# Performance work log

Measured on AMD Instinct MI355X. Metric: run time of the kernel, lower is better.

Reference implementation:

```python
import jax, jax.numpy as jnp
import numpy as np

B, N, C_IN, C_OUT, K = 2, 2048, 64, 128, 3
SCALE = 12.0  # spread points over ~12^3 unit voxels (voxel_size = 1.0 in the module)


def setup_inputs() -> dict:
    key = jax.random.key(0)
    k1, k2, k3 = jax.random.split(key, 3)
    points = jax.random.uniform(k1, (B, N, 3), dtype=jnp.float32) * SCALE
    features = jax.random.normal(k2, (B, N, C_IN), dtype=jnp.float32)
    # kaiming-uniform-ish init for weight viewed as (K^3*Cin, Cout)
    fan_in = K * K * K * C_IN
    bound = np.sqrt(6.0 / fan_in)
    weight = jax.random.uniform(k3, (K, K, K, C_IN, C_OUT), dtype=jnp.float32,
                                minval=-bound, maxval=bound)
    bias = jnp.zeros((C_OUT,), dtype=jnp.float32)
    return {"points": points, "features": features, "weight": weight, "bias": bias}


def reference(points, features, weight, bias):
    """Sparse 3D conv over a unit voxel grid.

    For each point i, every point j whose voxel index differs by an offset
    within the KxKxK stencil contributes features[j] @ weight[rel_offset].
    Vectorized as: per-offset boolean match matrix (B,N,N) -> masked
    feature aggregation -> one GEMM with that offset's (Cin,Cout) kernel slice.
    """
    k = weight.shape[0]
    c = k // 2
    # torch's .long() truncates toward zero; jnp astype(int32) does the same for floats
    vox = points.astype(jnp.int32)  # (B, N, 3)
    out = jnp.zeros(features.shape[:2] + (weight.shape[-1],), dtype=features.dtype)
    for oi in range(k):
        for oj in range(k):
            for ok in range(k):
                off = jnp.array([oi - c, oj - c, ok - c], dtype=jnp.int32)
                target = vox + off  # voxel that neighbor j must occupy for center i
                # mask[b, i, j] = all(vox[b, j] == vox[b, i] + off)
                mask = jnp.all(vox[:, None, :, :] == target[:, :, None, :], axis=-1)
                agg = jnp.einsum('bij,bjc->bic', mask.astype(features.dtype), features)
                out = out + agg @ weight[oi, oj, ok]  # (B,N,Cin)@(Cin,Cout)
    return out + bias
```

## Files before the change

kernel.cpp:

```cpp
#include <hip/hip_runtime.h>

#define BATCH 2
#define NPTS  2048
#define CIN   64
#define COUT  128
#define GD    14
#define GD2   (GD*GD)
#define NCELL (GD*GD*GD)
#define M     (BATCH*NPTS)
#define VOXF  (BATCH*NCELL*CIN)
#define WTEL  (27*COUT*CIN)

typedef __bf16 bf16x8 __attribute__((ext_vector_type(8)));
typedef float  f32x4  __attribute__((ext_vector_type(4)));
typedef unsigned short us8 __attribute__((ext_vector_type(8)));

__device__ __forceinline__ unsigned short f2bf(float f) {
    unsigned u = __builtin_bit_cast(unsigned, f);
    return (unsigned short)((u + 0x7FFFu + ((u >> 16) & 1u)) >> 16);
}

__global__ __launch_bounds__(256) void k_init(const float* __restrict__ points,
                                              const float* __restrict__ weight,
                                              int* __restrict__ abase,
                                              unsigned short* __restrict__ wT) {
    const int t = threadIdx.x;
    if (blockIdx.x < 27) {
        const int off = blockIdx.x;
        __shared__ unsigned short lds[128*65 + 64];
        const float* wsrc = weight + off*8192;
        #pragma unroll
        for (int i = 0; i < 32; ++i) {
            const int s = t + i*256;
            const int k = s >> 7, n = s & 127;
            lds[n*65 + k] = f2bf(wsrc[k*128 + n]);
        }
        __syncthreads();
        unsigned short* wdst = wT + off*8192;
        #pragma unroll
        for (int i = 0; i < 32; ++i) {
            const int s = t + i*256;
            const int n = s >> 6, k = s & 63;
            wdst[n*64 + k] = lds[n*65 + k];
        }
    } else {
        const int g = (blockIdx.x - 27)*256 + t;
        const int vx = (int)points[g*3 + 0];
        const int vy = (int)points[g*3 + 1];
        const int vz = (int)points[g*3 + 2];
        const int cell = (vx + 1)*GD2 + (vy + 1)*GD + (vz + 1);
        abase[g] = ((g >> 11)*NCELL + cell)*CIN;
    }
}

__global__ __launch_bounds__(256) void k_scatter(const float* __restrict__ feat,
                                                 const int* __restrict__ abase,
                                                 float* __restrict__ voxgrid) {
    const int idx = blockIdx.x * 256 + threadIdx.x;
    const int g   = idx >> 6;
    const int cin = idx & 63;
    atomicAdd(&voxgrid[abase[g] + cin], feat[idx]);
}

__global__ __launch_bounds__(256) void k_pack(const float* __restrict__ voxgrid,
                                              unsigned short* __restrict__ voxbf) {
    const int idx = blockIdx.x * 256 + threadIdx.x;
    if (idx >= VOXF/8) return;
    const float4 v0 = ((const float4*)voxgrid)[idx*2 + 0];
    const float4 v1 = ((const float4*)voxgrid)[idx*2 + 1];
    us8 p;
    p[0] = f2bf(v0.x); p[1] = f2bf(v0.y); p[2] = f2bf(v0.z); p[3] = f2bf(v0.w);
    p[4] = f2bf(v1.x); p[5] = f2bf(v1.y); p[6] = f2bf(v1.z); p[7] = f2bf(v1.w);
    *(us8*)(voxbf + idx*8) = p;
}

__global__ __launch_bounds__(256) void k_gemm(const unsigned short* __restrict__ voxbf,
                                              const int* __restrict__ abase,
                                              const unsigned short* __restrict__ wT,
                                              const float* __restrict__ bias,
                                              float* __restrict__ out) {
    static constexpr int DELTA[27] = {
        -211,-210,-209,-197,-196,-195,-183,-182,-181,
         -15, -14, -13,  -1,   0,   1,  13,  14,  15,
         181, 182, 183, 195, 196, 197, 209, 210, 211 };

    const int t   = threadIdx.x;
    const int l   = t & 63;
    const int w   = t >> 6;
    const int q   = l >> 4;
    const int col = l & 15;
    const int g0  = blockIdx.x * 16;
    const int n0  = (blockIdx.y * 4 + w) * 16;

    const int rowoff = abase[g0 + col];
    const unsigned short* arow = voxbf + rowoff + q*8;
    const unsigned short* wtp  = wT + (size_t)(n0 + col)*CIN + q*8;

    f32x4 acc = {0.f, 0.f, 0.f, 0.f};

    us8 A0[3], A1[3], B0[3], B1[3];
    #pragma unroll
    for (int p = 0; p < 3; ++p) {
        const int d = DELTA[p]*CIN;
        A0[p] = *(const us8*)(arow + d);
        A1[p] = *(const us8*)(arow + d + 32);
        B0[p] = *(const us8*)(wtp + p*8192);
        B1[p] = *(const us8*)(wtp + p*8192 + 32);
    }

    #pragma unroll
    for (int oo = 0; oo < 27; ++oo) {
        const int s = oo % 3;
        const us8 a0 = A0[s], a1 = A1[s], b0 = B0[s], b1 = B1[s];
        if (oo + 3 < 27) {
            const int d = DELTA[oo+3]*CIN;
            A0[s] = *(const us8*)(arow + d);
            A1[s] = *(const us8*)(arow + d + 32);
            B0[s] = *(const us8*)(wtp + (oo+3)*8192);
            B1[s] = *(const us8*)(wtp + (oo+3)*8192 + 32);
        }
        acc = __builtin_amdgcn_mfma_f32_16x16x32_bf16(
                  __builtin_bit_cast(bf16x8, a0), __builtin_bit_cast(bf16x8, b0), acc, 0, 0, 0);
        acc = __builtin_amdgcn_mfma_f32_16x16x32_bf16(
                  __builtin_bit_cast(bf16x8, a1), __builtin_bit_cast(bf16x8, b1), acc, 0, 0, 0);
    }

    const float bs = bias[n0 + col];
    #pragma unroll
    for (int r = 0; r < 4; ++r) {
        out[(size_t)(g0 + q*4 + r)*COUT + n0 + col] = acc[r] + bs;
    }
}

extern "C" void kernel_launch(void* const* d_in, const int* in_sizes, int n_in,
                              void* d_out, int out_size, void* d_ws, size_t ws_size,
                              hipStream_t stream) {
    (void)in_sizes; (void)n_in; (void)out_size; (void)ws_size;
    const float* points   = (const float*)d_in[0];
    const float* features = (const float*)d_in[1];
    const float* weight   = (const float*)d_in[2];
    const float* bias     = (const float*)d_in[3];
    float* out = (float*)d_out;

    char* ws = (char*)d_ws;
    float*          voxgrid = (float*)ws;
    int*            abase   = (int*)(ws + 1404928);
    unsigned short* wTp     = (unsigned short*)(ws + 1404928 + 16384);
    unsigned short* voxbf   = (unsigned short*)(ws + 1404928 + 16384 + 442368);

    hipMemsetAsync(voxgrid, 0, (size_t)VOXF*4, stream);
    k_init<<<43, 256, 0, stream>>>(points, weight, abase, wTp);
    k_scatter<<<(M*CIN)/256, 256, 0, stream>>>(features, abase, voxgrid);
    k_pack<<<(VOXF/8 + 255)/256, 256, 0, stream>>>(voxgrid, voxbf);
    dim3 grid(M/16, 2, 1);
    k_gemm<<<grid, 256, 0, stream>>>(voxbf, abase, wTp, bias, out);
}
```

Baseline: 94.87 us.

## Compute conv per voxel cell then gather to points; fuse init and scatter

The GEMM now runs over all 2x1728 occupied-range voxel cells instead of over the 4096 points, writes a dense per-cell output grid, and a new gather kernel copies each point's cell row to the output. The weight is re-laid-out so that the three z-offsets of a stencil row form one contiguous 192-wide K dimension. This lets the A loads for those offsets come from contiguous voxel memory. The separate init and scatter kernels are merged into one prep kernel to save a launch. The trade-off is fewer GEMM rows (3456 vs 4096) in exchange for an extra gather kernel and an extra intermediate buffer round trip.

```diff
diff --git a/kernel.cpp b/kernel.cpp
--- a/kernel.cpp
+++ b/kernel.cpp
@@ -9,7 +9,7 @@
 #define NCELL (GD*GD*GD)
 #define M     (BATCH*NPTS)
 #define VOXF  (BATCH*NCELL*CIN)
-#define WTEL  (27*COUT*CIN)
+#define MCELL (BATCH*1728)
 
 typedef __bf16 bf16x8 __attribute__((ext_vector_type(8)));
 typedef float  f32x4  __attribute__((ext_vector_type(4)));
@@ -20,46 +20,42 @@
     return (unsigned short)((u + 0x7FFFu + ((u >> 16) & 1u)) >> 16);
 }
 
-__global__ __launch_bounds__(256) void k_init(const float* __restrict__ points,
+__global__ __launch_bounds__(256) void k_prep(const float* __restrict__ points,
+                                              const float* __restrict__ features,
                                               const float* __restrict__ weight,
-                                              int* __restrict__ abase,
-                                              unsigned short* __restrict__ wT) {
+                                              float* __restrict__ voxgrid,
+                                              unsigned short* __restrict__ wT2) {
     const int t = threadIdx.x;
-    if (blockIdx.x < 27) {
-        const int off = blockIdx.x;
-        __shared__ unsigned short lds[128*65 + 64];
-        const float* wsrc = weight + off*8192;
+    if (blockIdx.x < 18) {
+        const int p  = blockIdx.x >> 1;
+        const int nh = blockIdx.x & 1;
+        __shared__ unsigned short lds[64*194];
         #pragma unroll
-        for (int i = 0; i < 32; ++i) {
-            const int s = t + i*256;
-            const int k = s >> 7, n = s & 127;
-            lds[n*65 + k] = f2bf(wsrc[k*128 + n]);
+        for (int i = 0; i < 48; ++i) {
+            const int s  = t + i*256;
+            const int nn = s & 63;
+            const int kk = s >> 6;
+            const int ok = kk >> 6, k = kk & 63;
+            lds[nn*194 + kk] = f2bf(weight[(p*3 + ok)*8192 + k*128 + nh*64 + nn]);
         }
         __syncthreads();
-        unsigned short* wdst = wT + off*8192;
         #pragma unroll
-        for (int i = 0; i < 32; ++i) {
-            const int s = t + i*256;
-            const int n = s >> 6, k = s & 63;
-            wdst[n*64 + k] = lds[n*65 + k];
+        for (int i = 0; i < 48; ++i) {
+            const int s  = t + i*256;
+            const int nn = s / 192;
+            const int kk = s - nn*192;
+            wT2[(size_t)(p*128 + nh*64 + nn)*192 + kk] = lds[nn*194 + kk];
         }
     } else {
-        const int g = (blockIdx.x - 27)*256 + t;
+        const int idx = (blockIdx.x - 18)*256 + t;
+        const int g   = idx >> 6;
+        const int cin = idx & 63;
         const int vx = (int)points[g*3 + 0];
         const int vy = (int)points[g*3 + 1];
         const int vz = (int)points[g*3 + 2];
         const int cell = (vx + 1)*GD2 + (vy + 1)*GD + (vz + 1);
-        abase[g] = ((g >> 11)*NCELL + cell)*CIN;
+        atomicAdd(&voxgrid[((size_t)(g >> 11)*NCELL + cell)*CIN + cin], features[idx]);
     }
-}
-
-__global__ __launch_bounds__(256) void k_scatter(const float* __restrict__ feat,
-                                                 const int* __restrict__ abase,
-                                                 float* __restrict__ voxgrid) {
-    const int idx = blockIdx.x * 256 + threadIdx.x;
-    const int g   = idx >> 6;
-    const int cin = idx & 63;
-    atomicAdd(&voxgrid[abase[g] + cin], feat[idx]);
 }
 
 __global__ __launch_bounds__(256) void k_pack(const float* __restrict__ voxgrid,
@@ -74,62 +70,71 @@
     *(us8*)(voxbf + idx*8) = p;
 }
 
-__global__ __launch_bounds__(256) void k_gemm(const unsigned short* __restrict__ voxbf,
-                                              const int* __restrict__ abase,
-                                              const unsigned short* __restrict__ wT,
+__global__ __launch_bounds__(256) void k_conv(const unsigned short* __restrict__ voxbf,
+                                              const unsigned short* __restrict__ wT2,
                                               const float* __restrict__ bias,
-                                              float* __restrict__ out) {
-    static constexpr int DELTA[27] = {
-        -211,-210,-209,-197,-196,-195,-183,-182,-181,
-         -15, -14, -13,  -1,   0,   1,  13,  14,  15,
-         181, 182, 183, 195, 196, 197, 209, 210, 211 };
+                                              float* __restrict__ outgrid) {
+    static constexpr int DOFF[9] = { -13504, -12608, -11712,
+                                       -960,    -64,    832,
+                                      11584,  12480,  13376 };
 
-    const int t   = threadIdx.x;
-    const int l   = t & 63;
-    const int w   = t >> 6;
-    const int q   = l >> 4;
-    const int col = l & 15;
-    const int g0  = blockIdx.x * 16;
-    const int n0  = (blockIdx.y * 4 + w) * 16;
+    const int t    = threadIdx.x;
+    const int l    = t & 63;
+    const int w    = t >> 6;
+    const int q    = l >> 4;
+    const int col  = l & 15;
+    const int mblk = blockIdx.x;
+    const int b    = (mblk >= 108);
+    const int ci0  = (mblk - b*108) * 16;
+    const int n0   = blockIdx.y*64 + w*16;
 
-    const int rowoff = abase[g0 + col];
-    const unsigned short* arow = voxbf + rowoff + q*8;
-    const unsigned short* wtp  = wT + (size_t)(n0 + col)*CIN + q*8;
+    const int ci = ci0 + col;
+    const int cx = ci / 144, cy = (ci / 12) % 12, cz = ci % 12;
+    const int v  = (cx + 1)*GD2 + (cy + 1)*GD + (cz + 1);
+    const unsigned short* aptr = voxbf + (size_t)(b*NCELL + v)*64 + q*8;
+    const unsigned short* bptr = wT2 + (size_t)(n0 + col)*192 + q*8;
 
     f32x4 acc = {0.f, 0.f, 0.f, 0.f};
 
-    us8 A0[3], A1[3], B0[3], B1[3];
+    us8 Ab[4], Bb[4];
     #pragma unroll
-    for (int p = 0; p < 3; ++p) {
-        const int d = DELTA[p]*CIN;
-        A0[p] = *(const us8*)(arow + d);
-        A1[p] = *(const us8*)(arow + d + 32);
-        B0[p] = *(const us8*)(wtp + p*8192);
-        B1[p] = *(const us8*)(wtp + p*8192 + 32);
+    for (int st = 0; st < 4; ++st) {
+        const int p = st / 6, s = st % 6;
+        Ab[st] = *(const us8*)(aptr + DOFF[p] + s*32);
+        Bb[st] = *(const us8*)(bptr + p*24576 + s*32);
     }
-
     #pragma unroll
-    for (int oo = 0; oo < 27; ++oo) {
-        const int s = oo % 3;
-        const us8 a0 = A0[s], a1 = A1[s], b0 = B0[s], b1 = B1[s];
-        if (oo + 3 < 27) {
-            const int d = DELTA[oo+3]*CIN;
-            A0[s] = *(const us8*)(arow + d);
-            A1[s] = *(const us8*)(arow + d + 32);
-            B0[s] = *(const us8*)(wtp + (oo+3)*8192);
-            B1[s] = *(const us8*)(wtp + (oo+3)*8192 + 32);
+    for (int st = 0; st < 54; ++st) {
+        const int sl = st & 3;
+        const us8 a = Ab[sl], bb = Bb[sl];
+        if (st + 4 < 54) {
+            const int p = (st + 4) / 6, s = (st + 4) % 6;
+            Ab[sl] = *(const us8*)(aptr + DOFF[p] + s*32);
+            Bb[sl] = *(const us8*)(bptr + p*24576 + s*32);
         }
         acc = __builtin_amdgcn_mfma_f32_16x16x32_bf16(
-                  __builtin_bit_cast(bf16x8, a0), __builtin_bit_cast(bf16x8, b0), acc, 0, 0, 0);
-        acc = __builtin_amdgcn_mfma_f32_16x16x32_bf16(
-                  __builtin_bit_cast(bf16x8, a1), __builtin_bit_cast(bf16x8, b1), acc, 0, 0, 0);
+                  __builtin_bit_cast(bf16x8, a), __builtin_bit_cast(bf16x8, bb), acc, 0, 0, 0);
     }
 
     const float bs = bias[n0 + col];
     #pragma unroll
     for (int r = 0; r < 4; ++r) {
-        out[(size_t)(g0 + q*4 + r)*COUT + n0 + col] = acc[r] + bs;
+        outgrid[(size_t)(mblk*16 + q*4 + r)*128 + n0 + col] = acc[r] + bs;
     }
+}
+
+__global__ __launch_bounds__(256) void k_gather(const float* __restrict__ points,
+                                                const float* __restrict__ outgrid,
+                                                float* __restrict__ out) {
+    const int idx = blockIdx.x * 256 + threadIdx.x;
+    const int g   = idx >> 5;
+    const int c4  = idx & 31;
+    const int vx = (int)points[g*3 + 0];
+    const int vy = (int)points[g*3 + 1];
+    const int vz = (int)points[g*3 + 2];
+    const int ci = vx*144 + vy*12 + vz;
+    const int mg = (g >> 11)*1728 + ci;
+    ((float4*)out)[(size_t)g*32 + c4] = ((const float4*)outgrid)[(size_t)mg*32 + c4];
 }
 
 extern "C" void kernel_launch(void* const* d_in, const int* in_sizes, int n_in,
@@ -144,14 +149,14 @@
 
     char* ws = (char*)d_ws;
     float*          voxgrid = (float*)ws;
-    int*            abase   = (int*)(ws + 1404928);
-    unsigned short* wTp     = (unsigned short*)(ws + 1404928 + 16384);
-    unsigned short* voxbf   = (unsigned short*)(ws + 1404928 + 16384 + 442368);
+    unsigned short* voxbf   = (unsigned short*)(ws + 1404928);
+    unsigned short* wT2     = (unsigned short*)(ws + 1404928 + 702464);
+    float*          outgrid = (float*)(ws + 1404928 + 702464 + 442368);
 
     hipMemsetAsync(voxgrid, 0, (size_t)VOXF*4, stream);
-    k_init<<<43, 256, 0, stream>>>(points, weight, abase, wTp);
-    k_scatter<<<(M*CIN)/256, 256, 0, stream>>>(features, abase, voxgrid);
+    k_prep<<<18 + (M*CIN)/256, 256, 0, stream>>>(points, features, weight, voxgrid, wT2);
     k_pack<<<(VOXF/8 + 255)/256, 256, 0, stream>>>(voxgrid, voxbf);
-    dim3 grid(M/16, 2, 1);
-    k_gemm<<<grid, 256, 0, stream>>>(voxbf, abase, wTp, bias, out);
+    dim3 cgrid(MCELL/16, 2, 1);
+    k_conv<<<cgrid, 256, 0, stream>>>(voxbf, wT2, bias, outgrid);
+    k_gather<<<(M*32)/256, 256, 0, stream>>>(points, outgrid, out);
 }
```

Result: no change. 96.37 us (+1.6%).
